# Kernel optimization log

Hardware: AMD Instinct MI355X
Metric: run time of the kernel (lower is better)

Reference implementation:

```python
import jax, jax.numpy as jnp
import numpy as np


def setup_inputs() -> dict:
    key = jax.random.key(0)
    k1, k2 = jax.random.split(key)
    x = jax.random.normal(k1, (4, 1, 16384), dtype=jnp.float32)  # [B, C, T]
    # dictionary initialized uniform(-1, 1) as in nn.Parameter(...).uniform_(-1, 1)
    d = jax.random.uniform(k2, (256, 1, 256), dtype=jnp.float32, minval=-1.0, maxval=1.0)  # [A, C, K]
    return {"x": x, "d": d, "n_iterations": 16}


def reference(x, d, n_iterations):
    B, C, T = x.shape
    A, _, K = d.shape
    pad = K // 2
    # normalize each atom over (channels, atom_size) dims, i.e. d_normalization_dims=(-1,-2)
    norms = jnp.linalg.norm(d.reshape(A, -1), axis=-1)
    dn = d / (norms[:, None, None] + 1e-12)

    # work in a padded domain so conv output position == start index in padded residual
    rp = jnp.pad(x, ((0, 0), (0, 0), (pad, pad)))        # residual, [B, C, T+2*pad]
    recon = jnp.zeros_like(rp)                            # accumulated reconstruction
    Tout = T + 2 * pad - K + 1                            # conv output length

    def step(carry, _):
        rp, recon = carry
        # cross-correlation of residual with every atom: [B, A, Tout]
        fm = jax.lax.conv_general_dilated(
            rp, dn, window_strides=(1,), padding='VALID',
            dimension_numbers=('NCH', 'OIH', 'NCH'))
        flat = fm.reshape(B, A * Tout)
        idx = jnp.argmax(flat, axis=-1)                   # signed max, per batch item
        val = jnp.take_along_axis(flat, idx[:, None], axis=-1)[:, 0]
        atom_idx = idx // Tout
        pos = idx % Tout                                  # start index in padded domain
        atoms = dn[atom_idx] * val[:, None, None]         # [B, C, K]

        def upd(r, rec, a, p):
            seg = jax.lax.dynamic_slice(r, (0, p), (C, K))
            r2 = jax.lax.dynamic_update_slice(r, seg - a, (0, p))
            segr = jax.lax.dynamic_slice(rec, (0, p), (C, K))
            rec2 = jax.lax.dynamic_update_slice(rec, segr + a, (0, p))
            return r2, rec2

        rp2, recon2 = jax.vmap(upd)(rp, recon, atoms, pos)
        return (rp2, recon2), None

    (rp, recon), _ = jax.lax.scan(step, (rp, recon), None, length=n_iterations)
    # crop padding -> reconstruction with same shape as x
    return recon[:, :, pad:pad + T]
```

## Files before the change

kernel.cpp:

```cpp
#include <hip/hip_runtime.h>
#include <math.h>

#define B    4
#define T    16384
#define A    256
#define K    256
#define PAD  128
#define TP   (T + 2*PAD)
#define TOUT (TP - K + 1)
#define ITERS 16
#define CHUNK 512
#define NCHUNK 33
#define NCP  36
#define TILE 2048
#define NTILE 9
#define NBLK 512
#define BPB2 128
#define HBASE 8192
#define RPSTORE 8448
#define RPN 8704
#define NGRP 8
#define SUBSTRIDE 32
#define BARSTRIDE (NGRP*SUBSTRIDE)
#define GSTRIDE 16
#define GPAR (NGRP*GSTRIDE)
#define DLDS 40960

#define TAP(acc, s0,s1,s2,s3, dq) { acc = fmaf(s0,(dq).x,acc); acc = fmaf(s1,(dq).y,acc); \
                                    acc = fmaf(s2,(dq).z,acc); acc = fmaf(s3,(dq).w,acc); }

typedef unsigned long long u64;

__device__ __forceinline__ void wave_amax(float& bv, int& bi) {
    #pragma unroll
    for (int off = 32; off; off >>= 1) {
        float ov = __shfl_down(bv, off);
        int   oi = __shfl_down(bi, off);
        if (ov > bv || (ov == bv && oi < bi)) { bv = ov; bi = oi; }
    }
}

struct KSmem {
    float  rp[RPN];
    float4 dn4[4][64];
    float  chv[4][34];
    int    chi[4][34];
    float  wv[16]; int wi[16];
    float  fv; int fi;
};

__device__ __forceinline__ void gbar_sub(unsigned* sub, int r, unsigned gen16, int tid) {
    __syncthreads();
    if (tid == 0)
        __hip_atomic_fetch_add(&sub[(r >> 4)*SUBSTRIDE], 1u,
                               __ATOMIC_RELEASE, __HIP_MEMORY_SCOPE_AGENT);
    if (tid < 64) {
        for (;;) {
            unsigned ok = 1;
            if (tid < NGRP)
                ok = (__hip_atomic_load(&sub[tid*SUBSTRIDE], __ATOMIC_RELAXED,
                                        __HIP_MEMORY_SCOPE_AGENT) >= gen16);
            if (__all((int)ok)) break;
            __builtin_amdgcn_s_sleep(4);
        }
    }
    __syncthreads();
    __builtin_amdgcn_fence(__ATOMIC_ACQUIRE, "agent");
}

__device__ void chunks_update(KSmem& sm, int baseF, int cA, int cB, int aBase, int tid) {
    const int lane = tid & 63, w = tid >> 6;
    const int grp = tid >> 7;
    const int cg = grp ? cB : cA;
    const int lt = cg*512 + (tid & 127)*4;
    float c0[4] = {0,0,0,0}, c1[4] = {0,0,0,0}, c2[4] = {0,0,0,0}, c3[4] = {0,0,0,0};
    if (cg >= 0) {
        const float4* srp4 = (const float4*)sm.rp;
        int ol4 = (lt - baseF) >> 2;
        float4 p = srp4[ol4];
        #pragma unroll 4
        for (int kq = 0; kq < 64; kq++) {
            float4 d0 = sm.dn4[0][kq];
            float4 d1 = sm.dn4[1][kq];
            float4 d2 = sm.dn4[2][kq];
            float4 d3 = sm.dn4[3][kq];
            float4 pn = srp4[ol4 + kq + 1];
            TAP(c0[0], p.x,p.y,p.z,p.w, d0); TAP(c0[1], p.y,p.z,p.w,pn.x, d0);
            TAP(c0[2], p.z,p.w,pn.x,pn.y, d0); TAP(c0[3], p.w,pn.x,pn.y,pn.z, d0);
            TAP(c1[0], p.x,p.y,p.z,p.w, d1); TAP(c1[1], p.y,p.z,p.w,pn.x, d1);
            TAP(c1[2], p.z,p.w,pn.x,pn.y, d1); TAP(c1[3], p.w,pn.x,pn.y,pn.z, d1);
            TAP(c2[0], p.x,p.y,p.z,p.w, d2); TAP(c2[1], p.y,p.z,p.w,pn.x, d2);
            TAP(c2[2], p.z,p.w,pn.x,pn.y, d2); TAP(c2[3], p.w,pn.x,pn.y,pn.z, d2);
            TAP(c3[0], p.x,p.y,p.z,p.w, d3); TAP(c3[1], p.y,p.z,p.w,pn.x, d3);
            TAP(c3[2], p.z,p.w,pn.x,pn.y, d3); TAP(c3[3], p.w,pn.x,pn.y,pn.z, d3);
            p = pn;
        }
    }
    float bv0 = -INFINITY, bv1 = -INFINITY, bv2 = -INFINITY, bv3 = -INFINITY;
    int bi0 = 0x7fffffff, bi1 = 0x7fffffff, bi2 = 0x7fffffff, bi3 = 0x7fffffff;
    if (cg >= 0) {
        #pragma unroll
        for (int j = 0; j < 4; j++) {
            int t = lt + j;
            if (t < TOUT) {
                if (c0[j] > bv0) { bv0 = c0[j]; bi0 = (aBase+0)*TOUT + t; }
                if (c1[j] > bv1) { bv1 = c1[j]; bi1 = (aBase+1)*TOUT + t; }
                if (c2[j] > bv2) { bv2 = c2[j]; bi2 = (aBase+2)*TOUT + t; }
                if (c3[j] > bv3) { bv3 = c3[j]; bi3 = (aBase+3)*TOUT + t; }
            }
        }
    }
    wave_amax(bv0, bi0); wave_amax(bv1, bi1); wave_amax(bv2, bi2); wave_amax(bv3, bi3);
    if (lane == 0) {
        sm.wv[0*4+w] = bv0; sm.wi[0*4+w] = bi0;
        sm.wv[1*4+w] = bv1; sm.wi[1*4+w] = bi1;
        sm.wv[2*4+w] = bv2; sm.wi[2*4+w] = bi2;
        sm.wv[3*4+w] = bv3; sm.wi[3*4+w] = bi3;
    }
    __syncthreads();
    if (tid < 8) {
        int a = tid >> 1, hh = tid & 1;
        int chunk = hh ? cB : cA;
        if (chunk >= 0) {
            float v0 = sm.wv[a*4 + 2*hh];   int i0 = sm.wi[a*4 + 2*hh];
            float v1 = sm.wv[a*4 + 2*hh+1]; int i1 = sm.wi[a*4 + 2*hh+1];
            if (v1 > v0 || (v1 == v0 && i1 < i0)) { v0 = v1; i0 = i1; }
            sm.chv[a][chunk] = v0; sm.chi[a][chunk] = i0;
        }
    }
    __syncthreads();
}

__device__ __forceinline__ void publish(KSmem& sm, u64* gslot, unsigned* gcnt,
                                        int gen, int h, int tid) {
    const int lane = tid & 63, w = tid >> 6;
    int cstart = h ? 16 : 0, nch = h ? 17 : 16;
    float bv = -INFINITY; int bi = 0x7fffffff;
    if (lane < nch) { bv = sm.chv[w][cstart + lane]; bi = sm.chi[w][cstart + lane]; }
    wave_amax(bv, bi);
    if (lane == 0) { sm.wv[8+w] = bv; sm.wi[8+w] = bi; }
    __syncthreads();
    if (tid == 0) {
        float v = sm.wv[8]; int i = sm.wi[8];
        #pragma unroll
        for (int j = 1; j < 4; j++)
            if (sm.wv[8+j] > v || (sm.wv[8+j] == v && sm.wi[8+j] < i)) { v = sm.wv[8+j]; i = sm.wi[8+j]; }
        unsigned s = __float_as_uint(v);
        unsigned key = (s & 0x80000000u) ? ~s : (s | 0x80000000u);
        u64 e = ((u64)(unsigned)gen << 55) | ((u64)key << 23)
              | (u64)(unsigned)(0x7FFFFF - i);
        __hip_atomic_fetch_max(gslot, e, __ATOMIC_RELAXED, __HIP_MEMORY_SCOPE_AGENT);
        asm volatile("s_waitcnt vmcnt(0)" ::: "memory");
        __hip_atomic_fetch_add(gcnt, 1u, __ATOMIC_RELAXED, __HIP_MEMORY_SCOPE_AGENT);
    }
}

__device__ __forceinline__ void pick(KSmem& sm, const u64* gparity,
                                     const unsigned* cntb, int gen, int tid) {
    const int lane = tid & 63;
    if (tid < 64) {
        for (;;) {
            unsigned ok = 1;
            if (lane < NGRP)
                ok = (__hip_atomic_load(&cntb[lane*SUBSTRIDE], __ATOMIC_RELAXED,
                                        __HIP_MEMORY_SCOPE_AGENT) >= (unsigned)gen*16u);
            if (__all((int)ok)) break;
            __builtin_amdgcn_s_sleep(2);
        }
        u64 e = 0;
        if (lane < NGRP) {
            const u64* p = gparity + lane*GSTRIDE;
            for (;;) {
                e = __hip_atomic_load(p, __ATOMIC_RELAXED, __HIP_MEMORY_SCOPE_AGENT);
                if ((unsigned)(e >> 55) == (unsigned)gen) break;
                __builtin_amdgcn_s_sleep(1);
            }
        }
        #pragma unroll
        for (int off = 4; off; off >>= 1) {
            u64 o = __shfl_down(e, off);
            if (lane < NGRP && o > e) e = o;
        }
        if (lane == 0) {
            unsigned key = (unsigned)((e >> 23) & 0xFFFFFFFFull);
            unsigned s = (key & 0x80000000u) ? (key ^ 0x80000000u) : ~key;
            sm.fv = __uint_as_float(s);
            sm.fi = 0x7FFFFF - (int)(e & 0x7FFFFF);
        }
    }
    __syncthreads();
}

__global__ void __launch_bounds__(256, 2)
k_coop(const float* __restrict__ x, const float* __restrict__ d, float* __restrict__ out,
       float* __restrict__ dn, u64* __restrict__ gmax,
       unsigned* __restrict__ cnt, unsigned* __restrict__ fbar) {
    extern __shared__ char raw[];
    KSmem& sm = *(KSmem*)raw;
    const int bid = blockIdx.x, tid = threadIdx.x;
    const int b = bid >> 7, r = bid & 127;
    const int h = r >> 6, a0 = r & 63;
    const int lane = tid & 63, w = tid >> 6;
    const int baseF = h * HBASE;
    const int cstart = h ? 16 : 0, cend = h ? 33 : 16;
    const int grp = r >> 4;
    u64* gmaxb = gmax + (size_t)b*2*GPAR;
    unsigned* cntb = cnt + b*BARSTRIDE;
    unsigned* fbarb = fbar + b*BARSTRIDE;

    {
        const float4* x4 = (const float4*)(x + (size_t)b*T);
        float4* rp4w = (float4*)sm.rp;
        int b4 = baseF >> 2;
        for (int i = tid; i < RPN/4; i += 256) {
            int g4 = b4 + i;
            float4 v = {0.f,0.f,0.f,0.f};
            if (i < RPSTORE/4 && g4 >= PAD/4 && g4 < (PAD+T)/4) v = x4[g4 - PAD/4];
            rp4w[i] = v;
        }
    }
    #pragma unroll
    for (int s = 0; s < 4; s++) {
        int atom = a0*4 + s;
        float v = d[atom*K + tid];
        float sq = v*v;
        #pragma unroll
        for (int off = 32; off; off >>= 1) sq += __shfl_down(sq, off);
        if (lane == 0) sm.wv[w] = sq;
        __syncthreads();
        float norm = sqrtf(sm.wv[0] + sm.wv[1] + sm.wv[2] + sm.wv[3]) + 1e-12f;
        float nv = v / norm;
        ((float*)&sm.dn4[s][0])[tid] = nv;
        dn[atom*K + tid] = nv;
        __syncthreads();
    }
    {
        int npass = h ? 9 : 8;
        for (int p = 0; p < npass; p++) {
            int ca = cstart + 2*p;
            int cb2 = (ca + 1 < cend) ? ca + 1 : -1;
            chunks_update(sm, baseF, ca, cb2, a0*4, tid);
        }
    }
    int gen = 1;
    publish(sm, gmaxb + (gen&1)*GPAR + grp*GSTRIDE, cntb + grp*SUBSTRIDE, gen, h, tid);
    gbar_sub(fbarb, r, 16u, tid);

    for (int it = 0; it < ITERS-1; it++) {
        pick(sm, gmaxb + (gen&1)*GPAR, cntb, gen, tid);
        float val = sm.fv; int idx = sm.fi;
        int atom = idx / TOUT, pos = idx - atom*TOUT;
        float ds = dn[atom*K + tid];
        int li = pos + tid - baseF;
        if (li >= 0 && li < RPSTORE) sm.rp[li] -= val * ds;
        __syncthreads();
        int lo = pos - (K-1); if (lo < 0) lo = 0;
        int g0 = lo >> 9, g1 = g0 + 1;
        bool in0 = (g0 >= cstart && g0 < cend);
        bool in1 = (g1 >= cstart && g1 < cend);
        int ca = in0 ? g0 : (in1 ? g1 : -1);
        int cb2 = (in0 && in1) ? g1 : -1;
        if (ca >= 0) chunks_update(sm, baseF, ca, cb2, a0*4, tid);
        publish(sm, gmaxb + ((gen+1)&1)*GPAR + grp*GSTRIDE, cntb + grp*SUBSTRIDE,
                gen+1, h, tid);
        gen++;
    }
    if (a0 == 0) {
        pick(sm, gmaxb + (gen&1)*GPAR, cntb, gen, tid);
        float val = sm.fv; int idx = sm.fi;
        int atom = idx / TOUT, pos = idx - atom*TOUT;
        float ds = dn[atom*K + tid];
        int li = pos + tid - baseF;
        if (li >= 0 && li < RPSTORE) sm.rp[li] -= val * ds;
        __syncthreads();
        int o_lo4 = h ? (HBASE - PAD)/4 : 0;
        int o_hi4 = h ? T/4 : (HBASE - PAD)/4;
        const float4* xb4 = (const float4*)(x + (size_t)b*T);
        float4* o4 = (float4*)(out + (size_t)b*T);
        for (int i4 = o_lo4 + tid; i4 < o_hi4; i4 += 256) {
            float4 xv = xb4[i4];
            float4 rv = *(const float4*)&sm.rp[i4*4 + PAD - baseF];
            float4 ov; ov.x = xv.x - rv.x; ov.y = xv.y - rv.y;
            ov.z = xv.z - rv.z; ov.w = xv.w - rv.w;
            o4[i4] = ov;
        }
    }
}

struct Smem {
    float rp[TILE + K + 16];
    float dnA[K];
    float dnB[K];
    float dnsel[K];
    float wv[16]; int wi[16];
    float fv; int fi;
};

__device__ __forceinline__ void dev_norm(int a0, int tid, const float* __restrict__ d,
                                         float* __restrict__ dn, Smem& sm) {
    int lane = tid & 63, w = tid >> 6;
    #pragma unroll
    for (int s = 0; s < 2; s++) {
        int atom = a0*2 + s;
        float v = d[atom*K + tid];
        float sq = v*v;
        #pragma unroll
        for (int off = 32; off; off >>= 1) sq += __shfl_down(sq, off);
        if (lane == 0) sm.wv[w] = sq;
        __syncthreads();
        float norm = sqrtf(sm.wv[0] + sm.wv[1] + sm.wv[2] + sm.wv[3]) + 1e-12f;
        dn[atom*K + tid] = v / norm;
        __syncthreads();
    }
}

__device__ __forceinline__ void dev_init(int a0, int b, int tid, const float* __restrict__ x,
                                         float* __restrict__ rp, float* __restrict__ recon) {
    int i = a0*256 + tid;
    if (i < TP) {
        float v = (i >= PAD && i < PAD + T) ? x[b*T + (i - PAD)] : 0.f;
        rp[(size_t)b*TP + i] = v;
        recon[(size_t)b*TP + i] = 0.f;
    }
}

__device__ void dev_conv(int a0, int b, int tid, const float* __restrict__ rp,
                         const float* __restrict__ dn,
                         float* __restrict__ segval, int* __restrict__ segidx,
                         float* __restrict__ abv, int* __restrict__ abi, Smem& sm) {
    const int aA = a0*2, aB = a0*2 + 1;
    const int lane = tid & 63, w = tid >> 6;
    sm.dnA[tid] = dn[aA*K + tid];
    sm.dnB[tid] = dn[aB*K + tid];
    const float4* rp4 = (const float4*)(rp + (size_t)b*TP);

    for (int tile = 0; tile < NTILE; tile++) {
        int t0 = tile * TILE;
        __syncthreads();
        float4* s4 = (float4*)sm.rp;
        for (int i = tid; i < 580; i += 256) {
            int g = t0/4 + i;
            float4 v = {0.f,0.f,0.f,0.f};
            if (g*4 < TP) v = rp4[g];
            s4[i] = v;
        }
        __syncthreads();
        const float4* srp4 = (const float4*)sm.rp;
        const float4* dA4  = (const float4*)sm.dnA;
        const float4* dB4  = (const float4*)sm.dnB;
        float accA0[4] = {0,0,0,0}, accA1[4] = {0,0,0,0};
        float accB0[4] = {0,0,0,0}, accB1[4] = {0,0,0,0};
        float4 p = srp4[tid];
        float4 q = srp4[tid + 256];
        #pragma unroll 4
        for (int kq = 0; kq < 64; kq++) {
            float4 dA = dA4[kq];
            float4 dB = dB4[kq];
            float4 pn = srp4[tid + kq + 1];
            float4 qn = srp4[tid + 256 + kq + 1];
            TAP(accA0[0], p.x,p.y,p.z,p.w, dA); TAP(accA0[1], p.y,p.z,p.w,pn.x, dA);
            TAP(accA0[2], p.z,p.w,pn.x,pn.y, dA); TAP(accA0[3], p.w,pn.x,pn.y,pn.z, dA);
            TAP(accB0[0], p.x,p.y,p.z,p.w, dB); TAP(accB0[1], p.y,p.z,p.w,pn.x, dB);
            TAP(accB0[2], p.z,p.w,pn.x,pn.y, dB); TAP(accB0[3], p.w,pn.x,pn.y,pn.z, dB);
            TAP(accA1[0], q.x,q.y,q.z,q.w, dA); TAP(accA1[1], q.y,q.z,q.w,qn.x, dA);
            TAP(accA1[2], q.z,q.w,qn.x,qn.y, dA); TAP(accA1[3], q.w,qn.x,qn.y,qn.z, dA);
            TAP(accB1[0], q.x,q.y,q.z,q.w, dB); TAP(accB1[1], q.y,q.z,q.w,qn.x, dB);
            TAP(accB1[2], q.z,q.w,qn.x,qn.y, dB); TAP(accB1[3], q.w,qn.x,qn.y,qn.z, dB);
            p = pn; q = qn;
        }
        int lt = tid * 4;
        float bvA0 = -INFINITY, bvA1 = -INFINITY, bvB0 = -INFINITY, bvB1 = -INFINITY;
        int biA0 = 0x7fffffff, biA1 = 0x7fffffff, biB0 = 0x7fffffff, biB1 = 0x7fffffff;
        #pragma unroll
        for (int j = 0; j < 4; j++) {
            int t = t0 + lt + j;
            if (t < TOUT) {
                if (accA0[j] > bvA0) { bvA0 = accA0[j]; biA0 = aA*TOUT + t; }
                if (accB0[j] > bvB0) { bvB0 = accB0[j]; biB0 = aB*TOUT + t; }
            }
            int t1 = t0 + 1024 + lt + j;
            if (t1 < TOUT) {
                if (accA1[j] > bvA1) { bvA1 = accA1[j]; biA1 = aA*TOUT + t1; }
                if (accB1[j] > bvB1) { bvB1 = accB1[j]; biB1 = aB*TOUT + t1; }
            }
        }
        wave_amax(bvA0, biA0); wave_amax(bvA1, biA1);
        wave_amax(bvB0, biB0); wave_amax(bvB1, biB1);
        if (lane == 0) {
            sm.wv[w]    = bvA0; sm.wi[w]    = biA0;
            sm.wv[4+w]  = bvA1; sm.wi[4+w]  = biA1;
            sm.wv[8+w]  = bvB0; sm.wi[8+w]  = biB0;
            sm.wv[12+w] = bvB1; sm.wi[12+w] = biB1;
        }
        __syncthreads();
        if (tid < 4) {
            float v0 = sm.wv[2*tid];   int i0 = sm.wi[2*tid];
            float v1 = sm.wv[2*tid+1]; int i1 = sm.wi[2*tid+1];
            if (v1 > v0 || (v1 == v0 && i1 < i0)) { v0 = v1; i0 = i1; }
            int chunk = tile*4 + tid;
            if (chunk < NCHUNK) {
                segval[((size_t)b*A + aA)*NCP + chunk] = v0;
                segidx[((size_t)b*A + aA)*NCP + chunk] = i0;
            }
        } else if (tid >= 64 && tid < 68) {
            int c = tid - 64;
            float v0 = sm.wv[8+2*c];   int i0 = sm.wi[8+2*c];
            float v1 = sm.wv[8+2*c+1]; int i1 = sm.wi[8+2*c+1];
            if (v1 > v0 || (v1 == v0 && i1 < i0)) { v0 = v1; i0 = i1; }
            int chunk = tile*4 + c;
            if (chunk < NCHUNK) {
                segval[((size_t)b*A + aB)*NCP + chunk] = v0;
                segidx[((size_t)b*A + aB)*NCP + chunk] = i0;
            }
        }
    }
    __syncthreads();
    if (w < 2) {
        int atom = (w == 0) ? aA : aB;
        float bv = -INFINITY; int bi = 0x7fffffff;
        if (lane < NCHUNK) {
            bv = segval[((size_t)b*A + atom)*NCP + lane];
            bi = segidx[((size_t)b*A + atom)*NCP + lane];
        }
        wave_amax(bv, bi);
        if (lane == 0) { abv[b*A + atom] = bv; abi[b*A + atom] = bi; }
    }
}

__device__ void dev_iter(int a0, int b, int tid, int last,
                         const float* __restrict__ avc, const int* __restrict__ aic,
                         float* __restrict__ avn, int* __restrict__ ain,
                         const float* __restrict__ rin, float* __restrict__ rout,
                         float* __restrict__ recon, const float* __restrict__ dn,
                         float* __restrict__ segval, int* __restrict__ segidx, Smem& sm) {
    const int aA = a0*2, aB = a0*2 + 1;
    const int lane = tid & 63, w = tid >> 6;

    float bv0 = avc[b*A + tid]; int bi0 = aic[b*A + tid];
    const float4* rin4 = (const float4*)(rin + (size_t)b*TP);
    const int icopy = a0*256 + tid;
    const bool docopy = (!last) && (icopy < TP/4);
    float4 vcopy = {0.f,0.f,0.f,0.f};
    if (docopy) vcopy = rin4[icopy];
    sm.dnA[tid] = dn[aA*K + tid];
    sm.dnB[tid] = dn[aB*K + tid];

    {
        float bv = bv0; int bi = bi0;
        wave_amax(bv, bi);
        if (lane == 0) { sm.wv[w] = bv; sm.wi[w] = bi; }
        __syncthreads();
        if (tid == 0) {
            bv = sm.wv[0]; bi = sm.wi[0];
            for (int j = 1; j < 4; j++)
                if (sm.wv[j] > bv || (sm.wv[j] == bv && sm.wi[j] < bi)) { bv = sm.wv[j]; bi = sm.wi[j]; }
            sm.fv = bv; sm.fi = bi;
        }
        __syncthreads();
    }
    float val = sm.fv; int idx = sm.fi;
    int atom = idx / TOUT, pos = idx - atom*TOUT;
    sm.dnsel[tid] = dn[atom*K + tid];

    int lo = pos - (K-1); if (lo < 0) lo = 0;
    int c_lo = lo >> 9;
    int tbase = c_lo * CHUNK;

    if (!last) {
        float4* s4 = (float4*)sm.rp;
        for (int i = tid; i < 324; i += 256) {
            int g = tbase/4 + i;
            float4 v = {0.f,0.f,0.f,0.f};
            if (g*4 < TP) v = rin4[g];
            s4[i] = v;
        }
    }
    __syncthreads();
    if (docopy) {
        float4* rout4 = (float4*)(rout + (size_t)b*TP);
        float4 v = vcopy;
        int o = icopy*4 - pos;
        if (o > -4 && o < K) {
            if (o+0 >= 0 && o+0 < K) v.x -= val * sm.dnsel[o+0];
            if (o+1 >= 0 && o+1 < K) v.y -= val * sm.dnsel[o+1];
            if (o+2 >= 0 && o+2 < K) v.z -= val * sm.dnsel[o+2];
            if (o+3 >= 0 && o+3 < K) v.w -= val * sm.dnsel[o+3];
        }
        rout4[icopy] = v;
    }
    if (a0 == 0) {
        recon[(size_t)b*TP + pos + tid] += val * sm.dnsel[tid];
    }
    if (last) return;

    sm.rp[pos + tid - tbase] -= val * sm.dnsel[tid];
    __syncthreads();

    const float4* srp4 = (const float4*)sm.rp;
    const float4* dA4  = (const float4*)sm.dnA;
    const float4* dB4  = (const float4*)sm.dnB;
    float cA[4] = {0,0,0,0}, cB[4] = {0,0,0,0};
    float4 p = srp4[tid];
    #pragma unroll 4
    for (int kq = 0; kq < 64; kq++) {
        float4 dA = dA4[kq];
        float4 dB = dB4[kq];
        float4 pn = srp4[tid + kq + 1];
        TAP(cA[0], p.x,p.y,p.z,p.w, dA); TAP(cA[1], p.y,p.z,p.w,pn.x, dA);
        TAP(cA[2], p.z,p.w,pn.x,pn.y, dA); TAP(cA[3], p.w,pn.x,pn.y,pn.z, dA);
        TAP(cB[0], p.x,p.y,p.z,p.w, dB); TAP(cB[1], p.y,p.z,p.w,pn.x, dB);
        TAP(cB[2], p.z,p.w,pn.x,pn.y, dB); TAP(cB[3], p.w,pn.x,pn.y,pn.z, dB);
        p = pn;
    }
    int lt = tid * 4;
    float bvA = -INFINITY, bvB = -INFINITY;
    int biA = 0x7fffffff, biB = 0x7fffffff;
    #pragma unroll
    for (int j = 0; j < 4; j++) {
        int t = tbase + lt + j;
        if (t < TOUT) {
            if (cA[j] > bvA) { bvA = cA[j]; biA = aA*TOUT + t; }
            if (cB[j] > bvB) { bvB = cB[j]; biB = aB*TOUT + t; }
        }
    }
    wave_amax(bvA, biA); wave_amax(bvB, biB);
    if (lane == 0) { sm.wv[w] = bvA; sm.wi[w] = biA; sm.wv[8+w] = bvB; sm.wi[8+w] = biB; }
    __syncthreads();
    if (tid < 2) {
        float v0 = sm.wv[2*tid];   int i0 = sm.wi[2*tid];
        float v1 = sm.wv[2*tid+1]; int i1 = sm.wi[2*tid+1];
        if (v1 > v0 || (v1 == v0 && i1 < i0)) { v0 = v1; i0 = i1; }
        int chunk = c_lo + tid;
        if (chunk < NCHUNK) {
            segval[((size_t)b*A + aA)*NCP + chunk] = v0;
            segidx[((size_t)b*A + aA)*NCP + chunk] = i0;
        }
    } else if (tid >= 64 && tid < 66) {
        int c = tid - 64;
        float v0 = sm.wv[8+2*c];   int i0 = sm.wi[8+2*c];
        float v1 = sm.wv[8+2*c+1]; int i1 = sm.wi[8+2*c+1];
        if (v1 > v0 || (v1 == v0 && i1 < i0)) { v0 = v1; i0 = i1; }
        int chunk = c_lo + c;
        if (chunk < NCHUNK) {
            segval[((size_t)b*A + aB)*NCP + chunk] = v0;
            segidx[((size_t)b*A + aB)*NCP + chunk] = i0;
        }
    }
    __syncthreads();
    if (w < 2) {
        int at = (w == 0) ? aA : aB;
        float bv = -INFINITY; int bi = 0x7fffffff;
        if (lane < NCHUNK) {
            bv = segval[((size_t)b*A + at)*NCP + lane];
            bi = segidx[((size_t)b*A + at)*NCP + lane];
        }
        wave_amax(bv, bi);
        if (lane == 0) { avn[b*A + at] = bv; ain[b*A + at] = bi; }
    }
}

__global__ void __launch_bounds__(256) k_f_norm_init(const float* x, const float* d,
                                                     float* dn, float* rp0, float* recon) {
    __shared__ Smem sm;
    dev_norm(blockIdx.x & 127, threadIdx.x, d, dn, sm);
    dev_init(blockIdx.x & 127, blockIdx.x >> 7, threadIdx.x, x, rp0, recon);
}
__global__ void __launch_bounds__(256, 2) k_f_conv(const float* rp, const float* dn,
                                                   float* segval, int* segidx,
                                                   float* abv, int* abi) {
    __shared__ Smem sm;
    dev_conv(blockIdx.x & 127, blockIdx.x >> 7, threadIdx.x, rp, dn, segval, segidx, abv, abi, sm);
}
__global__ void __launch_bounds__(256, 2) k_f_iter(int last,
                                                   const float* avc, const int* aic,
                                                   float* avn, int* ain,
                                                   const float* rin, float* rout,
                                                   float* recon, const float* dn,
                                                   float* segval, int* segidx) {
    __shared__ Smem sm;
    dev_iter(blockIdx.x & 127, blockIdx.x >> 7, threadIdx.x, last,
             avc, aic, avn, ain, rin, rout, recon, dn, segval, segidx, sm);
}
__global__ void k_f_out(const float* recon, float* out) {
    int i = blockIdx.x * blockDim.x + threadIdx.x;
    if (i >= B*T) return;
    int b = i / T, t = i - b*T;
    out[i] = recon[(size_t)b*TP + PAD + t];
}

extern "C" void kernel_launch(void* const* d_in, const int* in_sizes, int n_in,
                              void* d_out, int out_size, void* d_ws, size_t ws_size,
                              hipStream_t stream) {
    const float* x = (const float*)d_in[0];
    const float* d = (const float*)d_in[1];
    float* out = (float*)d_out;

    float* ws     = (float*)d_ws;
    float* dn     = ws;
    float* rp0    = dn  + (size_t)A*K;
    float* rp1    = rp0 + (size_t)B*TP;
    float* recon  = rp1 + (size_t)B*TP;
    float* segval = recon + (size_t)B*TP;
    int*   segidx = (int*)(segval + (size_t)B*A*NCP);
    float* abv0   = (float*)(segidx + (size_t)B*A*NCP);
    float* abv1   = abv0 + (size_t)B*2*A;
    int*   abi0   = (int*)(abv1 + (size_t)B*2*A);
    int*   abi1   = abi0 + (size_t)B*2*A;
    unsigned* cnt = (unsigned*)(abi1 + (size_t)B*2*A);
    unsigned* fbar= cnt + (size_t)B*BARSTRIDE;
    u64*  gmax    = (u64*)(fbar + (size_t)B*BARSTRIDE);

    (void)hipFuncSetAttribute((const void*)k_coop,
                              hipFuncAttributeMaxDynamicSharedMemorySize, DLDS);
    int nb = 0, ncu = 0;
    hipError_t e1 = hipOccupancyMaxActiveBlocksPerMultiprocessor(&nb, (const void*)k_coop,
                                                                 256, DLDS);
    hipError_t e2 = hipDeviceGetAttribute(&ncu, hipDeviceAttributeMultiprocessorCount, 0);
    bool coop = (e1 == hipSuccess && e2 == hipSuccess && nb > 0 && ncu > 0 &&
                 (long)nb * ncu >= NBLK);
    if (coop) {
        size_t zbytes = (size_t)B*BARSTRIDE*4*2 + (size_t)B*2*GPAR*8;
        (void)hipMemsetAsync(cnt, 0, zbytes, stream);
        hipLaunchKernelGGL(k_coop, dim3(NBLK), dim3(256), DLDS, stream,
                           x, d, out, dn, gmax, cnt, fbar);
        return;
    }
    k_f_norm_init<<<NBLK, 256, 0, stream>>>(x, d, dn, rp0, recon);
    k_f_conv<<<NBLK, 256, 0, stream>>>(rp0, dn, segval, segidx, abv0, abi0);
    float* rbuf[2] = {rp0, rp1};
    float* av[2]   = {abv0, abv1};
    int*   ai[2]   = {abi0, abi1};
    for (int it = 0; it < ITERS; it++) {
        k_f_iter<<<NBLK, 256, 0, stream>>>(it == ITERS-1 ? 1 : 0,
                                           av[it & 1], ai[it & 1],
                                           av[(it + 1) & 1], ai[(it + 1) & 1],
                                           rbuf[it & 1], rbuf[(it + 1) & 1],
                                           recon, dn, segval, segidx);
    }
    k_f_out<<<(B*T + 255)/256, 256, 0, stream>>>(recon, out);
}
```

Baseline: 517.0 us.

## Replace atomic-max group reduction with leader-block reduce and relay broadcast

Each block now stores its generation-tagged candidate to its own slot with a plain atomic store, replacing the atomic fetch_max plus counter increment. One leader block per batch item polls all 128 slots, reduces them, and writes the winner to 8 relay words that the other blocks poll with a single thread. This drops contended atomics and the two-phase counter/parity wait. In exchange the leader becomes a serial hop on the critical path, adding one extra global round-trip of latency per iteration.

```diff
diff --git a/kernel.cpp b/kernel.cpp
--- a/kernel.cpp
+++ b/kernel.cpp
@@ -22,8 +22,7 @@
 #define NGRP 8
 #define SUBSTRIDE 32
 #define BARSTRIDE (NGRP*SUBSTRIDE)
-#define GSTRIDE 16
-#define GPAR (NGRP*GSTRIDE)
+#define RSTRIDE 16
 #define DLDS 40960
 
 #define TAP(acc, s0,s1,s2,s3, dq) { acc = fmaf(s0,(dq).x,acc); acc = fmaf(s1,(dq).y,acc); \
@@ -47,6 +46,7 @@
     int    chi[4][34];
     float  wv[16]; int wi[16];
     float  fv; int fi;
+    u64    red[2];
 };
 
 __device__ __forceinline__ void gbar_sub(unsigned* sub, int r, unsigned gen16, int tid) {
@@ -131,8 +131,7 @@
     __syncthreads();
 }
 
-__device__ __forceinline__ void publish(KSmem& sm, u64* gslot, unsigned* gcnt,
-                                        int gen, int h, int tid) {
+__device__ __forceinline__ void publish(KSmem& sm, u64* slot, int gen, int h, int tid) {
     const int lane = tid & 63, w = tid >> 6;
     int cstart = h ? 16 : 0, nch = h ? 17 : 16;
     float bv = -INFINITY; int bi = 0x7fffffff;
@@ -149,52 +148,63 @@
         unsigned key = (s & 0x80000000u) ? ~s : (s | 0x80000000u);
         u64 e = ((u64)(unsigned)gen << 55) | ((u64)key << 23)
               | (u64)(unsigned)(0x7FFFFF - i);
-        __hip_atomic_fetch_max(gslot, e, __ATOMIC_RELAXED, __HIP_MEMORY_SCOPE_AGENT);
-        asm volatile("s_waitcnt vmcnt(0)" ::: "memory");
-        __hip_atomic_fetch_add(gcnt, 1u, __ATOMIC_RELAXED, __HIP_MEMORY_SCOPE_AGENT);
-    }
-}
-
-__device__ __forceinline__ void pick(KSmem& sm, const u64* gparity,
-                                     const unsigned* cntb, int gen, int tid) {
-    const int lane = tid & 63;
-    if (tid < 64) {
+        __hip_atomic_store(slot, e, __ATOMIC_RELAXED, __HIP_MEMORY_SCOPE_AGENT);
+    }
+}
+
+__device__ __forceinline__ void lead_reduce(KSmem& sm, u64* slotsb, u64* relayb,
+                                            int gen, int tid) {
+    const int lane = tid & 63, w = tid >> 6;
+    if (tid < BPB2) {
+        const u64* p = slotsb + tid;
+        u64 e;
         for (;;) {
-            unsigned ok = 1;
-            if (lane < NGRP)
-                ok = (__hip_atomic_load(&cntb[lane*SUBSTRIDE], __ATOMIC_RELAXED,
-                                        __HIP_MEMORY_SCOPE_AGENT) >= (unsigned)gen*16u);
-            if (__all((int)ok)) break;
+            e = __hip_atomic_load(p, __ATOMIC_RELAXED, __HIP_MEMORY_SCOPE_AGENT);
+            if ((unsigned)(e >> 55) == (unsigned)gen) break;
+            __builtin_amdgcn_s_sleep(1);
+        }
+        #pragma unroll
+        for (int off = 32; off; off >>= 1) {
+            u64 o = __shfl_down(e, off);
+            if (o > e) e = o;
+        }
+        if (lane == 0) sm.red[w] = e;
+    }
+    __syncthreads();
+    if (tid == 0) {
+        u64 m = (sm.red[0] > sm.red[1]) ? sm.red[0] : sm.red[1];
+        #pragma unroll
+        for (int j = 0; j < NGRP; j++)
+            __hip_atomic_store(&relayb[j*RSTRIDE], m, __ATOMIC_RELAXED,
+                               __HIP_MEMORY_SCOPE_AGENT);
+        unsigned key = (unsigned)((m >> 23) & 0xFFFFFFFFull);
+        unsigned s = (key & 0x80000000u) ? (key ^ 0x80000000u) : ~key;
+        sm.fv = __uint_as_float(s);
+        sm.fi = 0x7FFFFF - (int)(m & 0x7FFFFF);
+    }
+    __syncthreads();
+}
+
+__device__ __forceinline__ void pick_relay(KSmem& sm, const u64* rl, int gen, int tid) {
+    if (tid == 0) {
+        u64 e;
+        for (;;) {
+            e = __hip_atomic_load(rl, __ATOMIC_RELAXED, __HIP_MEMORY_SCOPE_AGENT);
+            if ((unsigned)(e >> 55) == (unsigned)gen) break;
             __builtin_amdgcn_s_sleep(2);
         }
-        u64 e = 0;
-        if (lane < NGRP) {
-            const u64* p = gparity + lane*GSTRIDE;
-            for (;;) {
-                e = __hip_atomic_load(p, __ATOMIC_RELAXED, __HIP_MEMORY_SCOPE_AGENT);
-                if ((unsigned)(e >> 55) == (unsigned)gen) break;
-                __builtin_amdgcn_s_sleep(1);
-            }
-        }
-        #pragma unroll
-        for (int off = 4; off; off >>= 1) {
-            u64 o = __shfl_down(e, off);
-            if (lane < NGRP && o > e) e = o;
-        }
-        if (lane == 0) {
-            unsigned key = (unsigned)((e >> 23) & 0xFFFFFFFFull);
-            unsigned s = (key & 0x80000000u) ? (key ^ 0x80000000u) : ~key;
-            sm.fv = __uint_as_float(s);
-            sm.fi = 0x7FFFFF - (int)(e & 0x7FFFFF);
-        }
+        unsigned key = (unsigned)((e >> 23) & 0xFFFFFFFFull);
+        unsigned s = (key & 0x80000000u) ? (key ^ 0x80000000u) : ~key;
+        sm.fv = __uint_as_float(s);
+        sm.fi = 0x7FFFFF - (int)(e & 0x7FFFFF);
     }
     __syncthreads();
 }
 
 __global__ void __launch_bounds__(256, 2)
 k_coop(const float* __restrict__ x, const float* __restrict__ d, float* __restrict__ out,
-       float* __restrict__ dn, u64* __restrict__ gmax,
-       unsigned* __restrict__ cnt, unsigned* __restrict__ fbar) {
+       float* __restrict__ dn, u64* __restrict__ slots, u64* __restrict__ relay,
+       unsigned* __restrict__ fbar) {
     extern __shared__ char raw[];
     KSmem& sm = *(KSmem*)raw;
     const int bid = blockIdx.x, tid = threadIdx.x;
@@ -203,9 +213,9 @@
     const int lane = tid & 63, w = tid >> 6;
     const int baseF = h * HBASE;
     const int cstart = h ? 16 : 0, cend = h ? 33 : 16;
-    const int grp = r >> 4;
-    u64* gmaxb = gmax + (size_t)b*2*GPAR;
-    unsigned* cntb = cnt + b*BARSTRIDE;
+    const bool islead = (r == 0);
+    u64* slotsb = slots + (size_t)b*BPB2;
+    u64* relayb = relay + (size_t)b*NGRP*RSTRIDE;
     unsigned* fbarb = fbar + b*BARSTRIDE;
 
     {
@@ -243,11 +253,12 @@
         }
     }
     int gen = 1;
-    publish(sm, gmaxb + (gen&1)*GPAR + grp*GSTRIDE, cntb + grp*SUBSTRIDE, gen, h, tid);
+    publish(sm, slotsb + r, gen, h, tid);
     gbar_sub(fbarb, r, 16u, tid);
 
     for (int it = 0; it < ITERS-1; it++) {
-        pick(sm, gmaxb + (gen&1)*GPAR, cntb, gen, tid);
+        if (islead) lead_reduce(sm, slotsb, relayb, gen, tid);
+        else        pick_relay(sm, relayb + (r >> 4)*RSTRIDE, gen, tid);
         float val = sm.fv; int idx = sm.fi;
         int atom = idx / TOUT, pos = idx - atom*TOUT;
         float ds = dn[atom*K + tid];
@@ -261,12 +272,12 @@
         int ca = in0 ? g0 : (in1 ? g1 : -1);
         int cb2 = (in0 && in1) ? g1 : -1;
         if (ca >= 0) chunks_update(sm, baseF, ca, cb2, a0*4, tid);
-        publish(sm, gmaxb + ((gen+1)&1)*GPAR + grp*GSTRIDE, cntb + grp*SUBSTRIDE,
-                gen+1, h, tid);
+        publish(sm, slotsb + r, gen+1, h, tid);
         gen++;
     }
     if (a0 == 0) {
-        pick(sm, gmaxb + (gen&1)*GPAR, cntb, gen, tid);
+        if (islead) lead_reduce(sm, slotsb, relayb, gen, tid);
+        else        pick_relay(sm, relayb + (r >> 4)*RSTRIDE, gen, tid);
         float val = sm.fv; int idx = sm.fi;
         int atom = idx / TOUT, pos = idx - atom*TOUT;
         float ds = dn[atom*K + tid];
@@ -606,9 +617,9 @@
     float* abv1   = abv0 + (size_t)B*2*A;
     int*   abi0   = (int*)(abv1 + (size_t)B*2*A);
     int*   abi1   = abi0 + (size_t)B*2*A;
-    unsigned* cnt = (unsigned*)(abi1 + (size_t)B*2*A);
-    unsigned* fbar= cnt + (size_t)B*BARSTRIDE;
-    u64*  gmax    = (u64*)(fbar + (size_t)B*BARSTRIDE);
+    unsigned* fbar= (unsigned*)(abi1 + (size_t)B*2*A);
+    u64*  slots   = (u64*)(fbar + (size_t)B*BARSTRIDE);
+    u64*  relay   = slots + (size_t)B*BPB2;
 
     (void)hipFuncSetAttribute((const void*)k_coop,
                               hipFuncAttributeMaxDynamicSharedMemorySize, DLDS);
@@ -619,10 +630,11 @@
     bool coop = (e1 == hipSuccess && e2 == hipSuccess && nb > 0 && ncu > 0 &&
                  (long)nb * ncu >= NBLK);
     if (coop) {
-        size_t zbytes = (size_t)B*BARSTRIDE*4*2 + (size_t)B*2*GPAR*8;
-        (void)hipMemsetAsync(cnt, 0, zbytes, stream);
+        size_t zbytes = (size_t)B*BARSTRIDE*4 + (size_t)B*BPB2*8
+                      + (size_t)B*NGRP*RSTRIDE*8;
+        (void)hipMemsetAsync(fbar, 0, zbytes, stream);
         hipLaunchKernelGGL(k_coop, dim3(NBLK), dim3(256), DLDS, stream,
-                           x, d, out, dn, gmax, cnt, fbar);
+                           x, d, out, dn, slots, relay, fbar);
         return;
     }
     k_f_norm_init<<<NBLK, 256, 0, stream>>>(x, d, dn, rp0, recon);
```

Result: faster. 498.8 us (-3.5%).
